# Optimization experiments

Measured on AMD Instinct MI355X. Metric: run time of the kernel, lower is better.

The kernel has to match this reference:

```python
import jax, jax.numpy as jnp
import numpy as np

N_NODES = 50000
N_EDGES = 800000
NFEAT = 96
NHID = 96
NCLASS = 40


def setup_inputs() -> dict:
    key = jax.random.key(0)
    ks = jax.random.split(key, 8)
    x = jax.random.normal(ks[0], (N_NODES, NFEAT), dtype=jnp.float32)
    edge_index = jax.random.randint(ks[1], (2, N_EDGES), 0, N_NODES, dtype=jnp.int64)
    def glorot(k, shape):
        fan_in = shape[1]
        bound = 1.0 / np.sqrt(fan_in)
        return jax.random.uniform(k, shape, jnp.float32, -bound, bound)
    return {
        'x': x,
        'edge_index': edge_index,
        'W1_l': glorot(ks[2], (NHID, NFEAT)),
        'b1_l': jnp.zeros((NHID,), jnp.float32),
        'W1_r': glorot(ks[3], (NHID, NFEAT)),
        'W2_l': glorot(ks[4], (NCLASS, NHID)),
        'b2_l': jnp.zeros((NCLASS,), jnp.float32),
        'W2_r': glorot(ks[5], (NCLASS, NHID)),
    }


def _sage_conv(x, src, dst, W_l, b_l, W_r):
    # gather neighbor features per edge, scatter-mean onto dst nodes
    msg = x[src]                                   # [E, F]
    agg = jax.ops.segment_sum(msg, dst, num_segments=N_NODES)   # [N, F]
    cnt = jax.ops.segment_sum(jnp.ones((src.shape[0],), x.dtype), dst,
                              num_segments=N_NODES)             # [N]
    agg = agg / jnp.maximum(cnt, 1.0)[:, None]
    # lin_l(agg) + lin_r(x)
    return agg @ W_l.T + b_l + x @ W_r.T


def reference(x, edge_index, W1_l, b1_l, W1_r, W2_l, b2_l, W2_r):
    src, dst = edge_index[0], edge_index[1]
    h = _sage_conv(x, src, dst, W1_l, b1_l, W1_r)
    h = jax.nn.relu(h)  # dropout is identity in eval mode
    h = _sage_conv(h, src, dst, W2_l, b2_l, W2_r)
    return jax.nn.log_softmax(h, axis=1)
```

## Files before the change

### kernel.cpp

```cpp
#include <hip/hip_runtime.h>
#include <math.h>

#define NCLASS 40
#define BSH    6
#define BSIZE  64
#define MAXB   1024
#define EPB    4096
#define LCOL   2048

typedef __attribute__((ext_vector_type(8))) short short8;
typedef __attribute__((ext_vector_type(4))) float float4v;

__device__ __forceinline__ unsigned short f2bf(float f) {
    union { float f; unsigned u; } v; v.f = f;
    unsigned r = v.u + 0x7fffu + ((v.u >> 16) & 1u);
    return (unsigned short)(r >> 16);
}
__device__ __forceinline__ float bf2f(unsigned int s) {
    union { unsigned u; float f; } v; v.u = s << 16; return v.f;
}

__global__ __launch_bounds__(256) void conv_kernel(const float4* __restrict__ x4,
                                                   const float* __restrict__ W1l,
                                                   const float* __restrict__ W1r,
                                                   const float* __restrict__ W2l,
                                                   const float* __restrict__ W2r,
                                                   unsigned short* __restrict__ axb,
                                                   unsigned short* __restrict__ wb1,
                                                   unsigned short* __restrict__ wb2,
                                                   int N, int xblocks) {
    int tid = threadIdx.x;
    if ((int)blockIdx.x < xblocks) {
        int idx = blockIdx.x * 256 + tid;
        if (idx >= N * 24) return;
        int n = idx / 24, q = idx - n * 24;
        float4 v = x4[idx];
        ushort4 o;
        o.x = f2bf(v.x); o.y = f2bf(v.y); o.z = f2bf(v.z); o.w = f2bf(v.w);
        *(ushort4*)(axb + (size_t)n * 192 + 96 + q * 4) = o;
        return;
    }
    int t = (blockIdx.x - xblocks) * 256 + tid;
    const float* src;
    unsigned short* dst;
    if (t < 36 * 64) {
        int s = t >> 6, lane = t & 63;
        int kc = s / 6, jt = s - kc * 6;
        int j  = jt * 16 + (lane & 15);
        int k2 = kc * 32 + (lane >> 4) * 8;
        src = (k2 < 96) ? (W1l + j * 96 + k2) : (W1r + j * 96 + (k2 - 96));
        dst = wb1 + t * 8;
    } else if (t < 51 * 64) {
        int t2 = t - 36 * 64;
        int s = t2 >> 6, lane = t2 & 63;
        int kc = s / 5, jt = s - kc * 5;
        int j  = jt * 16 + (lane & 15);
        int k2 = kc * 32 + (lane >> 4) * 8;
        src = (j < 40) ? (W2l + j * 96 + k2) : (W2r + (j - 40) * 96 + k2);
        dst = wb2 + t2 * 8;
    } else return;
    ushort4 o0, o1;
    o0.x = f2bf(src[0]); o0.y = f2bf(src[1]); o0.z = f2bf(src[2]); o0.w = f2bf(src[3]);
    o1.x = f2bf(src[4]); o1.y = f2bf(src[5]); o1.z = f2bf(src[6]); o1.w = f2bf(src[7]);
    *(ushort4*)(dst)     = o0;
    *(ushort4*)(dst + 4) = o1;
}

__global__ __launch_bounds__(256) void bhist_kernel(const int* __restrict__ ei,
                                                    int* __restrict__ histT,
                                                    int E, int nbucket, int nbin) {
    __shared__ int hcnt[MAXB];
    int tid = threadIdx.x;
    for (int t = tid; t < nbucket; t += 256) hcnt[t] = 0;
    __syncthreads();
    int e0 = blockIdx.x * EPB;
    for (int it = 0; it < EPB / 256; ++it) {
        int e = e0 + it * 256 + tid;
        if (e < E) atomicAdd(&hcnt[ei[E + e] >> BSH], 1);
    }
    __syncthreads();
    for (int t = tid; t < nbucket; t += 256)
        histT[t * nbin + blockIdx.x] = hcnt[t];
}

__global__ __launch_bounds__(256) void bsum_kernel(int* __restrict__ histT,
                                                   int* __restrict__ gbh, int nbin) {
    __shared__ int s[256];
    int k = blockIdx.x, tid = threadIdx.x;
    int v = (tid < nbin) ? histT[k * nbin + tid] : 0;
    s[tid] = v;
    __syncthreads();
    for (int off = 1; off < 256; off <<= 1) {
        int o = (tid >= off) ? s[tid - off] : 0;
        __syncthreads();
        s[tid] += o;
        __syncthreads();
    }
    if (tid < nbin) histT[k * nbin + tid] = s[tid] - v;
    if (tid == 255) gbh[k] = s[255];
}

__global__ __launch_bounds__(256) void bscan_kernel(const int* __restrict__ gbh,
                                                    int* __restrict__ gbase,
                                                    int* __restrict__ rp,
                                                    int N, int E, int nbucket) {
    __shared__ int s[256];
    int tid  = threadIdx.x;
    int base = tid * 4;
    int w0 = (base     < nbucket) ? gbh[base]     : 0;
    int w1 = (base + 1 < nbucket) ? gbh[base + 1] : 0;
    int w2 = (base + 2 < nbucket) ? gbh[base + 2] : 0;
    int w3 = (base + 3 < nbucket) ? gbh[base + 3] : 0;
    int tsum = w0 + w1 + w2 + w3;
    s[tid] = tsum;
    __syncthreads();
    for (int off = 1; off < 256; off <<= 1) {
        int o = (tid >= off) ? s[tid - off] : 0;
        __syncthreads();
        s[tid] += o;
        __syncthreads();
    }
    int excl = s[tid] - tsum;
    if (base < nbucket) {
        gbase[base] = excl;
        if (base + 1 <= nbucket) gbase[base + 1] = excl + w0;
        if (base + 2 <= nbucket) gbase[base + 2] = excl + w0 + w1;
        if (base + 3 <= nbucket) gbase[base + 3] = excl + w0 + w1 + w2;
    }
    if (tid == 0) { gbase[nbucket] = E; rp[N] = E; }
}

__global__ __launch_bounds__(256) void bin_kernel(const int* __restrict__ ei,
                                                  const int* __restrict__ gbase,
                                                  const int* __restrict__ histT,
                                                  unsigned int* __restrict__ tmp,
                                                  int E, int nbucket, int nbin) {
    __shared__ int lcnt[MAXB];
    __shared__ int lbase[MAXB];
    int tid = threadIdx.x;
    for (int t = tid; t < nbucket; t += 256) {
        lbase[t] = gbase[t] + histT[t * nbin + blockIdx.x];
        lcnt[t]  = 0;
    }
    __syncthreads();
    int e0 = blockIdx.x * EPB;
    for (int it = 0; it < EPB / 256; ++it) {
        int e = e0 + it * 256 + tid;
        if (e < E) {
            int src = ei[e], dst = ei[E + e];
            int b   = dst >> BSH;
            int ofs = atomicAdd(&lcnt[b], 1);
            tmp[lbase[b] + ofs] = (unsigned)src | ((unsigned)(dst & (BSIZE - 1)) << 16);
        }
    }
}

__global__ __launch_bounds__(256) void csr_agg_kernel(const unsigned int* __restrict__ tmp,
                                                      const int* __restrict__ gbase,
                                                      int* __restrict__ rp,
                                                      unsigned short* __restrict__ col,
                                                      unsigned short* __restrict__ axb,
                                                      int N) {
    __shared__ int ncnt[BSIZE], nofs[BSIZE], sscan[BSIZE];
    __shared__ unsigned short lcol[LCOL];
    int b   = blockIdx.x;
    int tid = threadIdx.x;
    int s0 = gbase[b], s1 = gbase[b + 1];
    int cnt = s1 - s0;
    bool inl = (cnt <= LCOL);
    if (tid < BSIZE) ncnt[tid] = 0;
    __syncthreads();
    for (int i = s0 + tid; i < s1; i += 256)
        atomicAdd(&ncnt[tmp[i] >> 16], 1);
    __syncthreads();
    int v = (tid < BSIZE) ? ncnt[tid] : 0;
    if (tid < BSIZE) sscan[tid] = v;
    __syncthreads();
    for (int off = 1; off < BSIZE; off <<= 1) {
        int o = (tid < BSIZE && tid >= off) ? sscan[tid - off] : 0;
        __syncthreads();
        if (tid < BSIZE) sscan[tid] += o;
        __syncthreads();
    }
    if (tid < BSIZE) {
        nofs[tid] = sscan[tid] - v;
        int node = (b << BSH) + tid;
        if (node < N) rp[node] = s0 + nofs[tid];
        ncnt[tid] = 0;
    }
    __syncthreads();
    for (int i = s0 + tid; i < s1; i += 256) {
        unsigned int t2 = tmp[i];
        int d   = t2 >> 16;
        int ofs = atomicAdd(&ncnt[d], 1);
        int pos = nofs[d] + ofs;
        unsigned short sv = (unsigned short)(t2 & 0xffffu);
        col[s0 + pos] = sv;
        if (inl) lcol[pos] = sv;
    }
    __syncthreads();
    int nodebase = b << BSH;
    for (int item = tid; item < BSIZE * 12; item += 256) {
        int nl = item / 12;
        int q  = item - nl * 12;
        int ls  = nofs[nl];
        int deg = ncnt[nl];
        int le  = ls + deg;
        float a0=0.f,a1=0.f,a2=0.f,a3=0.f,a4=0.f,a5=0.f,a6=0.f,a7=0.f;
        int i = ls;
        for (; i + 3 < le; i += 4) {
            int c0 = inl ? lcol[i]   : col[s0 + i];
            int c1 = inl ? lcol[i+1] : col[s0 + i + 1];
            int c2 = inl ? lcol[i+2] : col[s0 + i + 2];
            int c3 = inl ? lcol[i+3] : col[s0 + i + 3];
            uint4 u0 = *(const uint4*)(axb + (size_t)c0 * 192 + 96 + q * 8);
            uint4 u1 = *(const uint4*)(axb + (size_t)c1 * 192 + 96 + q * 8);
            uint4 u2 = *(const uint4*)(axb + (size_t)c2 * 192 + 96 + q * 8);
            uint4 u3 = *(const uint4*)(axb + (size_t)c3 * 192 + 96 + q * 8);
            a0 += bf2f(u0.x & 0xffffu) + bf2f(u1.x & 0xffffu) + bf2f(u2.x & 0xffffu) + bf2f(u3.x & 0xffffu);
            a1 += bf2f(u0.x >> 16)     + bf2f(u1.x >> 16)     + bf2f(u2.x >> 16)     + bf2f(u3.x >> 16);
            a2 += bf2f(u0.y & 0xffffu) + bf2f(u1.y & 0xffffu) + bf2f(u2.y & 0xffffu) + bf2f(u3.y & 0xffffu);
            a3 += bf2f(u0.y >> 16)     + bf2f(u1.y >> 16)     + bf2f(u2.y >> 16)     + bf2f(u3.y >> 16);
            a4 += bf2f(u0.z & 0xffffu) + bf2f(u1.z & 0xffffu) + bf2f(u2.z & 0xffffu) + bf2f(u3.z & 0xffffu);
            a5 += bf2f(u0.z >> 16)     + bf2f(u1.z >> 16)     + bf2f(u2.z >> 16)     + bf2f(u3.z >> 16);
            a6 += bf2f(u0.w & 0xffffu) + bf2f(u1.w & 0xffffu) + bf2f(u2.w & 0xffffu) + bf2f(u3.w & 0xffffu);
            a7 += bf2f(u0.w >> 16)     + bf2f(u1.w >> 16)     + bf2f(u2.w >> 16)     + bf2f(u3.w >> 16);
        }
        for (; i < le; ++i) {
            int c = inl ? lcol[i] : col[s0 + i];
            uint4 u0 = *(const uint4*)(axb + (size_t)c * 192 + 96 + q * 8);
            a0 += bf2f(u0.x & 0xffffu); a1 += bf2f(u0.x >> 16);
            a2 += bf2f(u0.y & 0xffffu); a3 += bf2f(u0.y >> 16);
            a4 += bf2f(u0.z & 0xffffu); a5 += bf2f(u0.z >> 16);
            a6 += bf2f(u0.w & 0xffffu); a7 += bf2f(u0.w >> 16);
        }
        float inv = 1.0f / (float)(deg > 1 ? deg : 1);
        ushort4 o0, o1;
        o0.x = f2bf(a0 * inv); o0.y = f2bf(a1 * inv);
        o0.z = f2bf(a2 * inv); o0.w = f2bf(a3 * inv);
        o1.x = f2bf(a4 * inv); o1.y = f2bf(a5 * inv);
        o1.z = f2bf(a6 * inv); o1.w = f2bf(a7 * inv);
        *(ushort4*)(axb + (size_t)(nodebase + nl) * 192 + q * 8)     = o0;
        *(ushort4*)(axb + (size_t)(nodebase + nl) * 192 + q * 8 + 4) = o1;
    }
}

__global__ __launch_bounds__(256) void l1proj_kernel(const unsigned short* __restrict__ axb,
                                                     const unsigned short* __restrict__ wb1,
                                                     const float* __restrict__ b1,
                                                     const unsigned short* __restrict__ wb2,
                                                     unsigned short* __restrict__ pl,
                                                     float* __restrict__ pr,
                                                     int N) {
    __shared__ unsigned short sh[128 * 104];
    int wave = threadIdx.x >> 6, lane = threadIdx.x & 63;
    int nbase = blockIdx.x * 128 + wave * 32;
    int lbase = wave * 32;
    int mrow = lane & 15, quad = lane >> 4;

    {
        float4v acc[2][6] = {};
        const short8* W = (const short8*)wb1;
        #pragma unroll
        for (int kc = 0; kc < 6; ++kc) {
            short8 a0 = *(const short8*)(axb + (size_t)(nbase + mrow)      * 192 + kc * 32 + quad * 8);
            short8 a1 = *(const short8*)(axb + (size_t)(nbase + 16 + mrow) * 192 + kc * 32 + quad * 8);
            #pragma unroll
            for (int jt = 0; jt < 6; ++jt) {
                short8 b = W[(kc * 6 + jt) * 64 + lane];
                acc[0][jt] = __builtin_amdgcn_mfma_f32_16x16x32_bf16(a0, b, acc[0][jt], 0, 0, 0);
                acc[1][jt] = __builtin_amdgcn_mfma_f32_16x16x32_bf16(a1, b, acc[1][jt], 0, 0, 0);
            }
        }
        #pragma unroll
        for (int jt = 0; jt < 6; ++jt) {
            int j = jt * 16 + mrow;
            float bj = b1[j];
            #pragma unroll
            for (int mt = 0; mt < 2; ++mt) {
                #pragma unroll
                for (int r = 0; r < 4; ++r) {
                    int nl = lbase + mt * 16 + quad * 4 + r;
                    sh[nl * 104 + j] = f2bf(fmaxf(acc[mt][jt][r] + bj, 0.f));
                }
            }
        }
    }
    __syncthreads();
    {
        float4v acc[2][5] = {};
        const short8* W = (const short8*)wb2;
        #pragma unroll
        for (int kc = 0; kc < 3; ++kc) {
            short8 a0 = *(const short8*)&sh[(lbase + mrow)      * 104 + kc * 32 + quad * 8];
            short8 a1 = *(const short8*)&sh[(lbase + 16 + mrow) * 104 + kc * 32 + quad * 8];
            #pragma unroll
            for (int jt = 0; jt < 5; ++jt) {
                short8 b = W[(kc * 5 + jt) * 64 + lane];
                acc[0][jt] = __builtin_amdgcn_mfma_f32_16x16x32_bf16(a0, b, acc[0][jt], 0, 0, 0);
                acc[1][jt] = __builtin_amdgcn_mfma_f32_16x16x32_bf16(a1, b, acc[1][jt], 0, 0, 0);
            }
        }
        #pragma unroll
        for (int jt = 0; jt < 5; ++jt) {
            int j = jt * 16 + mrow;
            #pragma unroll
            for (int mt = 0; mt < 2; ++mt) {
                #pragma unroll
                for (int r = 0; r < 4; ++r) {
                    int node = nbase + mt * 16 + quad * 4 + r;
                    if (node < N) {
                        float v = acc[mt][jt][r];
                        if (j < 40) pl[(size_t)node * 64 + j] = f2bf(v);
                        else        pr[(size_t)node * 40 + (j - 40)] = v;
                    }
                }
            }
        }
    }
}

__global__ __launch_bounds__(256) void final_kernel(const unsigned short* __restrict__ pl,
                                                    const float* __restrict__ pr,
                                                    const float* __restrict__ b,
                                                    const int* __restrict__ rp,
                                                    const unsigned short* __restrict__ col,
                                                    float* __restrict__ out, int N) {
    int w    = threadIdx.x >> 6;
    int lane = threadIdx.x & 63;
    int n = blockIdx.x * 4 + w;
    if (n >= N) return;
    int s = rp[n], e = rp[n + 1];
    bool act = lane < NCLASS;
    float acc = 0.f;
    int i = s;
    for (; i + 7 < e; i += 8) {
        int c0 = col[i],   c1 = col[i+1], c2 = col[i+2], c3 = col[i+3];
        int c4 = col[i+4], c5 = col[i+5], c6 = col[i+6], c7 = col[i+7];
        if (act) {
            acc += bf2f(pl[(size_t)c0 * 64 + lane]) + bf2f(pl[(size_t)c1 * 64 + lane])
                 + bf2f(pl[(size_t)c2 * 64 + lane]) + bf2f(pl[(size_t)c3 * 64 + lane])
                 + bf2f(pl[(size_t)c4 * 64 + lane]) + bf2f(pl[(size_t)c5 * 64 + lane])
                 + bf2f(pl[(size_t)c6 * 64 + lane]) + bf2f(pl[(size_t)c7 * 64 + lane]);
        }
    }
    for (; i + 3 < e; i += 4) {
        int c0 = col[i], c1 = col[i+1], c2 = col[i+2], c3 = col[i+3];
        if (act) acc += bf2f(pl[(size_t)c0 * 64 + lane]) + bf2f(pl[(size_t)c1 * 64 + lane])
                      + bf2f(pl[(size_t)c2 * 64 + lane]) + bf2f(pl[(size_t)c3 * 64 + lane]);
    }
    for (; i < e; ++i) {
        int c = col[i];
        if (act) acc += bf2f(pl[(size_t)c * 64 + lane]);
    }
    float v = -INFINITY;
    if (act) {
        int deg = e - s;
        float inv = 1.0f / (float)(deg > 1 ? deg : 1);
        v = acc * inv + b[lane] + pr[(size_t)n * 40 + lane];
    }
    float m = v;
    #pragma unroll
    for (int off = 32; off >= 1; off >>= 1) m = fmaxf(m, __shfl_xor(m, off));
    float ex = act ? __expf(v - m) : 0.f;
    float ssum = ex;
    #pragma unroll
    for (int off = 32; off >= 1; off >>= 1) ssum += __shfl_xor(ssum, off);
    if (act) out[(size_t)n * 40 + lane] = v - m - __logf(ssum);
}

extern "C" void kernel_launch(void* const* d_in, const int* in_sizes, int n_in,
                              void* d_out, int out_size, void* d_ws, size_t ws_size,
                              hipStream_t stream) {
    const float* x   = (const float*)d_in[0];
    const int*   ei  = (const int*)  d_in[1];
    const float* W1l = (const float*)d_in[2];
    const float* b1  = (const float*)d_in[3];
    const float* W1r = (const float*)d_in[4];
    const float* W2l = (const float*)d_in[5];
    const float* b2  = (const float*)d_in[6];
    const float* W2r = (const float*)d_in[7];
    float* out = (float*)d_out;

    const int N = in_sizes[0] / 96;
    const int E = in_sizes[1] / 2;
    const int nbucket = (N + BSIZE - 1) >> BSH;
    const int nbin = (E + EPB - 1) / EPB;
    const int NB   = (N + 127) / 128;
    const int NP2  = NB * 128;
    const int xblocks = (N * 24 + 255) / 256;

    auto al = [](size_t v) { return (v + 255) & ~(size_t)255; };
    char* ws = (char*)d_ws;
    size_t o = 0;
    int* histT = (int*)(ws + o); o = al(o + (size_t)MAXB * 256 * 4);
    int* gbh   = (int*)(ws + o); o = al(o + (size_t)MAXB * 4);
    int* gbase = (int*)(ws + o); o = al(o + (size_t)(MAXB + 1) * 4);
    int* rp    = (int*)(ws + o); o = al(o + (size_t)(N + 1) * 4);
    unsigned int*   tmp = (unsigned int*)(ws + o);   o = al(o + (size_t)E * 4);
    unsigned short* col = (unsigned short*)(ws + o); o = al(o + (size_t)E * 2);
    unsigned short* axb = (unsigned short*)(ws + o); o = al(o + (size_t)NP2 * 192 * 2);
    unsigned short* wb1 = (unsigned short*)(ws + o); o = al(o + 36 * 64 * 8 * 2);
    unsigned short* wb2 = (unsigned short*)(ws + o); o = al(o + 15 * 64 * 8 * 2);
    unsigned short* pl  = (unsigned short*)(ws + o); o = al(o + (size_t)NP2 * 64 * 2);
    float*          pr  = (float*)(ws + o);          o = al(o + (size_t)N * 40 * 4);

    conv_kernel<<<xblocks + 13, 256, 0, stream>>>(
        (const float4*)x, W1l, W1r, W2l, W2r, axb, wb1, wb2, N, xblocks);
    bhist_kernel<<<nbin, 256, 0, stream>>>(ei, histT, E, nbucket, nbin);
    bsum_kernel <<<nbucket, 256, 0, stream>>>(histT, gbh, nbin);
    bscan_kernel<<<1, 256, 0, stream>>>(gbh, gbase, rp, N, E, nbucket);
    bin_kernel  <<<nbin, 256, 0, stream>>>(ei, gbase, histT, tmp, E, nbucket, nbin);
    csr_agg_kernel<<<nbucket, 256, 0, stream>>>(tmp, gbase, rp, col, axb, N);
    l1proj_kernel<<<NB, 256, 0, stream>>>(axb, wb1, b1, wb2, pl, pr, N);
    final_kernel<<<(N + 3) / 4, 256, 0, stream>>>(pl, pr, b2, rp, col, out, N);
}
```

Before: 182.0 us.

## Fuse histogram into convert kernel, restructure gathers, fold bias into projection

Merges the edge-bucket histogram kernel into the bf16 conversion kernel, saving one launch and letting the two independent phases run side by side. The layer-1 CSR gather now unrolls by 8, and its column source is hoisted out of the loop through a lambda specialisation. The final kernel splits each wave into 6 groups of 10 lanes, each lane loading 4 bf16 values. The groups cover different edges in parallel and are combined through shared memory, and the layer-2 bias is added during projection. This adds LDS traffic and leaves 4 lanes per wave idle, in exchange for more memory-level parallelism per node.

```diff
diff --git a/kernel.cpp b/kernel.cpp
--- a/kernel.cpp
+++ b/kernel.cpp
@@ -20,18 +20,36 @@
     union { unsigned u; float f; } v; v.u = s << 16; return v.f;
 }
 
-__global__ __launch_bounds__(256) void conv_kernel(const float4* __restrict__ x4,
-                                                   const float* __restrict__ W1l,
-                                                   const float* __restrict__ W1r,
-                                                   const float* __restrict__ W2l,
-                                                   const float* __restrict__ W2r,
-                                                   unsigned short* __restrict__ axb,
-                                                   unsigned short* __restrict__ wb1,
-                                                   unsigned short* __restrict__ wb2,
-                                                   int N, int xblocks) {
+__global__ __launch_bounds__(256) void convhist_kernel(const int* __restrict__ ei,
+                                                       const float4* __restrict__ x4,
+                                                       const float* __restrict__ W1l,
+                                                       const float* __restrict__ W1r,
+                                                       const float* __restrict__ W2l,
+                                                       const float* __restrict__ W2r,
+                                                       int* __restrict__ histT,
+                                                       unsigned short* __restrict__ axb,
+                                                       unsigned short* __restrict__ wb1,
+                                                       unsigned short* __restrict__ wb2,
+                                                       int N, int E, int nbucket,
+                                                       int nbin, int xblocks) {
+    __shared__ int hcnt[MAXB];
     int tid = threadIdx.x;
-    if ((int)blockIdx.x < xblocks) {
-        int idx = blockIdx.x * 256 + tid;
+    int blk = blockIdx.x;
+    if (blk < nbin) {
+        for (int t = tid; t < nbucket; t += 256) hcnt[t] = 0;
+        __syncthreads();
+        int e0 = blk * EPB;
+        for (int it = 0; it < EPB / 256; ++it) {
+            int e = e0 + it * 256 + tid;
+            if (e < E) atomicAdd(&hcnt[ei[E + e] >> BSH], 1);
+        }
+        __syncthreads();
+        for (int t = tid; t < nbucket; t += 256)
+            histT[t * nbin + blk] = hcnt[t];
+        return;
+    }
+    if (blk < nbin + xblocks) {
+        int idx = (blk - nbin) * 256 + tid;
         if (idx >= N * 24) return;
         int n = idx / 24, q = idx - n * 24;
         float4 v = x4[idx];
@@ -40,7 +58,7 @@
         *(ushort4*)(axb + (size_t)n * 192 + 96 + q * 4) = o;
         return;
     }
-    int t = (blockIdx.x - xblocks) * 256 + tid;
+    int t = (blk - nbin - xblocks) * 256 + tid;
     const float* src;
     unsigned short* dst;
     if (t < 36 * 64) {
@@ -66,23 +84,6 @@
     *(ushort4*)(dst + 4) = o1;
 }
 
-__global__ __launch_bounds__(256) void bhist_kernel(const int* __restrict__ ei,
-                                                    int* __restrict__ histT,
-                                                    int E, int nbucket, int nbin) {
-    __shared__ int hcnt[MAXB];
-    int tid = threadIdx.x;
-    for (int t = tid; t < nbucket; t += 256) hcnt[t] = 0;
-    __syncthreads();
-    int e0 = blockIdx.x * EPB;
-    for (int it = 0; it < EPB / 256; ++it) {
-        int e = e0 + it * 256 + tid;
-        if (e < E) atomicAdd(&hcnt[ei[E + e] >> BSH], 1);
-    }
-    __syncthreads();
-    for (int t = tid; t < nbucket; t += 256)
-        histT[t * nbin + blockIdx.x] = hcnt[t];
-}
-
 __global__ __launch_bounds__(256) void bsum_kernel(int* __restrict__ histT,
                                                    int* __restrict__ gbh, int nbin) {
     __shared__ int s[256];
@@ -200,55 +201,53 @@
     }
     __syncthreads();
     int nodebase = b << BSH;
-    for (int item = tid; item < BSIZE * 12; item += 256) {
-        int nl = item / 12;
-        int q  = item - nl * 12;
-        int ls  = nofs[nl];
-        int deg = ncnt[nl];
-        int le  = ls + deg;
-        float a0=0.f,a1=0.f,a2=0.f,a3=0.f,a4=0.f,a5=0.f,a6=0.f,a7=0.f;
-        int i = ls;
-        for (; i + 3 < le; i += 4) {
-            int c0 = inl ? lcol[i]   : col[s0 + i];
-            int c1 = inl ? lcol[i+1] : col[s0 + i + 1];
-            int c2 = inl ? lcol[i+2] : col[s0 + i + 2];
-            int c3 = inl ? lcol[i+3] : col[s0 + i + 3];
-            uint4 u0 = *(const uint4*)(axb + (size_t)c0 * 192 + 96 + q * 8);
-            uint4 u1 = *(const uint4*)(axb + (size_t)c1 * 192 + 96 + q * 8);
-            uint4 u2 = *(const uint4*)(axb + (size_t)c2 * 192 + 96 + q * 8);
-            uint4 u3 = *(const uint4*)(axb + (size_t)c3 * 192 + 96 + q * 8);
-            a0 += bf2f(u0.x & 0xffffu) + bf2f(u1.x & 0xffffu) + bf2f(u2.x & 0xffffu) + bf2f(u3.x & 0xffffu);
-            a1 += bf2f(u0.x >> 16)     + bf2f(u1.x >> 16)     + bf2f(u2.x >> 16)     + bf2f(u3.x >> 16);
-            a2 += bf2f(u0.y & 0xffffu) + bf2f(u1.y & 0xffffu) + bf2f(u2.y & 0xffffu) + bf2f(u3.y & 0xffffu);
-            a3 += bf2f(u0.y >> 16)     + bf2f(u1.y >> 16)     + bf2f(u2.y >> 16)     + bf2f(u3.y >> 16);
-            a4 += bf2f(u0.z & 0xffffu) + bf2f(u1.z & 0xffffu) + bf2f(u2.z & 0xffffu) + bf2f(u3.z & 0xffffu);
-            a5 += bf2f(u0.z >> 16)     + bf2f(u1.z >> 16)     + bf2f(u2.z >> 16)     + bf2f(u3.z >> 16);
-            a6 += bf2f(u0.w & 0xffffu) + bf2f(u1.w & 0xffffu) + bf2f(u2.w & 0xffffu) + bf2f(u3.w & 0xffffu);
-            a7 += bf2f(u0.w >> 16)     + bf2f(u1.w >> 16)     + bf2f(u2.w >> 16)     + bf2f(u3.w >> 16);
-        }
-        for (; i < le; ++i) {
-            int c = inl ? lcol[i] : col[s0 + i];
-            uint4 u0 = *(const uint4*)(axb + (size_t)c * 192 + 96 + q * 8);
-            a0 += bf2f(u0.x & 0xffffu); a1 += bf2f(u0.x >> 16);
-            a2 += bf2f(u0.y & 0xffffu); a3 += bf2f(u0.y >> 16);
-            a4 += bf2f(u0.z & 0xffffu); a5 += bf2f(u0.z >> 16);
-            a6 += bf2f(u0.w & 0xffffu); a7 += bf2f(u0.w >> 16);
-        }
-        float inv = 1.0f / (float)(deg > 1 ? deg : 1);
-        ushort4 o0, o1;
-        o0.x = f2bf(a0 * inv); o0.y = f2bf(a1 * inv);
-        o0.z = f2bf(a2 * inv); o0.w = f2bf(a3 * inv);
-        o1.x = f2bf(a4 * inv); o1.y = f2bf(a5 * inv);
-        o1.z = f2bf(a6 * inv); o1.w = f2bf(a7 * inv);
-        *(ushort4*)(axb + (size_t)(nodebase + nl) * 192 + q * 8)     = o0;
-        *(ushort4*)(axb + (size_t)(nodebase + nl) * 192 + q * 8 + 4) = o1;
-    }
+    auto gather = [&](auto getc) {
+        for (int item = tid; item < BSIZE * 12; item += 256) {
+            int nl = item / 12;
+            int q  = item - nl * 12;
+            int ls  = nofs[nl];
+            int deg = ncnt[nl];
+            int le  = ls + deg;
+            float a0=0.f,a1=0.f,a2=0.f,a3=0.f,a4=0.f,a5=0.f,a6=0.f,a7=0.f;
+            int i = ls;
+            for (; i + 7 < le; i += 8) {
+                #pragma unroll
+                for (int u = 0; u < 8; ++u) {
+                    int c = getc(i + u);
+                    uint4 w = *(const uint4*)(axb + (size_t)c * 192 + 96 + q * 8);
+                    a0 += bf2f(w.x & 0xffffu); a1 += bf2f(w.x >> 16);
+                    a2 += bf2f(w.y & 0xffffu); a3 += bf2f(w.y >> 16);
+                    a4 += bf2f(w.z & 0xffffu); a5 += bf2f(w.z >> 16);
+                    a6 += bf2f(w.w & 0xffffu); a7 += bf2f(w.w >> 16);
+                }
+            }
+            for (; i < le; ++i) {
+                int c = getc(i);
+                uint4 w = *(const uint4*)(axb + (size_t)c * 192 + 96 + q * 8);
+                a0 += bf2f(w.x & 0xffffu); a1 += bf2f(w.x >> 16);
+                a2 += bf2f(w.y & 0xffffu); a3 += bf2f(w.y >> 16);
+                a4 += bf2f(w.z & 0xffffu); a5 += bf2f(w.z >> 16);
+                a6 += bf2f(w.w & 0xffffu); a7 += bf2f(w.w >> 16);
+            }
+            float inv = 1.0f / (float)(deg > 1 ? deg : 1);
+            ushort4 o0, o1;
+            o0.x = f2bf(a0 * inv); o0.y = f2bf(a1 * inv);
+            o0.z = f2bf(a2 * inv); o0.w = f2bf(a3 * inv);
+            o1.x = f2bf(a4 * inv); o1.y = f2bf(a5 * inv);
+            o1.z = f2bf(a6 * inv); o1.w = f2bf(a7 * inv);
+            *(ushort4*)(axb + (size_t)(nodebase + nl) * 192 + q * 8)     = o0;
+            *(ushort4*)(axb + (size_t)(nodebase + nl) * 192 + q * 8 + 4) = o1;
+        }
+    };
+    if (inl) gather([&](int i) { return (int)lcol[i]; });
+    else     gather([&](int i) { return (int)col[s0 + i]; });
 }
 
 __global__ __launch_bounds__(256) void l1proj_kernel(const unsigned short* __restrict__ axb,
                                                      const unsigned short* __restrict__ wb1,
                                                      const float* __restrict__ b1,
                                                      const unsigned short* __restrict__ wb2,
+                                                     const float* __restrict__ b2,
                                                      unsigned short* __restrict__ pl,
                                                      float* __restrict__ pr,
                                                      int N) {
@@ -304,6 +303,7 @@
         #pragma unroll
         for (int jt = 0; jt < 5; ++jt) {
             int j = jt * 16 + mrow;
+            float b2v = (j >= 40) ? b2[j - 40] : 0.f;
             #pragma unroll
             for (int mt = 0; mt < 2; ++mt) {
                 #pragma unroll
@@ -312,7 +312,7 @@
                     if (node < N) {
                         float v = acc[mt][jt][r];
                         if (j < 40) pl[(size_t)node * 64 + j] = f2bf(v);
-                        else        pr[(size_t)node * 40 + (j - 40)] = v;
+                        else        pr[(size_t)node * 40 + (j - 40)] = v + b2v;
                     }
                 }
             }
@@ -322,42 +322,41 @@
 
 __global__ __launch_bounds__(256) void final_kernel(const unsigned short* __restrict__ pl,
                                                     const float* __restrict__ pr,
-                                                    const float* __restrict__ b,
                                                     const int* __restrict__ rp,
                                                     const unsigned short* __restrict__ col,
                                                     float* __restrict__ out, int N) {
-    int w    = threadIdx.x >> 6;
+    __shared__ float red[4][6][40];
+    int wave = threadIdx.x >> 6;
     int lane = threadIdx.x & 63;
-    int n = blockIdx.x * 4 + w;
+    int n = blockIdx.x * 4 + wave;
     if (n >= N) return;
     int s = rp[n], e = rp[n + 1];
-    bool act = lane < NCLASS;
-    float acc = 0.f;
-    int i = s;
-    for (; i + 7 < e; i += 8) {
-        int c0 = col[i],   c1 = col[i+1], c2 = col[i+2], c3 = col[i+3];
-        int c4 = col[i+4], c5 = col[i+5], c6 = col[i+6], c7 = col[i+7];
-        if (act) {
-            acc += bf2f(pl[(size_t)c0 * 64 + lane]) + bf2f(pl[(size_t)c1 * 64 + lane])
-                 + bf2f(pl[(size_t)c2 * 64 + lane]) + bf2f(pl[(size_t)c3 * 64 + lane])
-                 + bf2f(pl[(size_t)c4 * 64 + lane]) + bf2f(pl[(size_t)c5 * 64 + lane])
-                 + bf2f(pl[(size_t)c6 * 64 + lane]) + bf2f(pl[(size_t)c7 * 64 + lane]);
-        }
-    }
-    for (; i + 3 < e; i += 4) {
-        int c0 = col[i], c1 = col[i+1], c2 = col[i+2], c3 = col[i+3];
-        if (act) acc += bf2f(pl[(size_t)c0 * 64 + lane]) + bf2f(pl[(size_t)c1 * 64 + lane])
-                      + bf2f(pl[(size_t)c2 * 64 + lane]) + bf2f(pl[(size_t)c3 * 64 + lane]);
-    }
-    for (; i < e; ++i) {
-        int c = col[i];
-        if (act) acc += bf2f(pl[(size_t)c * 64 + lane]);
-    }
+    int g = lane / 10;
+    int c = lane - g * 10;
+    bool gok = (g < 6);
+    float a0 = 0.f, a1 = 0.f, a2 = 0.f, a3 = 0.f;
+    for (int base = s; base < e; base += 6) {
+        int idx = base + g;
+        if (gok && idx < e) {
+            int cn = col[idx];
+            uint2 u = *(const uint2*)(pl + (size_t)cn * 64 + c * 4);
+            a0 += bf2f(u.x & 0xffffu); a1 += bf2f(u.x >> 16);
+            a2 += bf2f(u.y & 0xffffu); a3 += bf2f(u.y >> 16);
+        }
+    }
+    if (gok) {
+        float4 t; t.x = a0; t.y = a1; t.z = a2; t.w = a3;
+        *(float4*)&red[wave][g][c * 4] = t;
+    }
+    bool act = (lane < NCLASS);
     float v = -INFINITY;
     if (act) {
+        float val = 0.f;
+        #pragma unroll
+        for (int gg = 0; gg < 6; ++gg) val += red[wave][gg][lane];
         int deg = e - s;
         float inv = 1.0f / (float)(deg > 1 ? deg : 1);
-        v = acc * inv + b[lane] + pr[(size_t)n * 40 + lane];
+        v = val * inv + pr[(size_t)n * 40 + lane];
     }
     float m = v;
     #pragma unroll
@@ -405,13 +404,13 @@
     unsigned short* pl  = (unsigned short*)(ws + o); o = al(o + (size_t)NP2 * 64 * 2);
     float*          pr  = (float*)(ws + o);          o = al(o + (size_t)N * 40 * 4);
 
-    conv_kernel<<<xblocks + 13, 256, 0, stream>>>(
-        (const float4*)x, W1l, W1r, W2l, W2r, axb, wb1, wb2, N, xblocks);
-    bhist_kernel<<<nbin, 256, 0, stream>>>(ei, histT, E, nbucket, nbin);
+    convhist_kernel<<<nbin + xblocks + 13, 256, 0, stream>>>(
+        ei, (const float4*)x, W1l, W1r, W2l, W2r, histT, axb, wb1, wb2,
+        N, E, nbucket, nbin, xblocks);
     bsum_kernel <<<nbucket, 256, 0, stream>>>(histT, gbh, nbin);
     bscan_kernel<<<1, 256, 0, stream>>>(gbh, gbase, rp, N, E, nbucket);
     bin_kernel  <<<nbin, 256, 0, stream>>>(ei, gbase, histT, tmp, E, nbucket, nbin);
     csr_agg_kernel<<<nbucket, 256, 0, stream>>>(tmp, gbase, rp, col, axb, N);
-    l1proj_kernel<<<NB, 256, 0, stream>>>(axb, wb1, b1, wb2, pl, pr, N);
-    final_kernel<<<(N + 3) / 4, 256, 0, stream>>>(pl, pr, b2, rp, col, out, N);
-}
+    l1proj_kernel<<<NB, 256, 0, stream>>>(axb, wb1, b1, wb2, b2, pl, pr, N);
+    final_kernel<<<(N + 3) / 4, 256, 0, stream>>>(pl, pr, rp, col, out, N);
+}
```

After: 179.3 us. Within noise of the previous version (-1.5%).
